# Kernel tuning notes

Hardware: AMD Instinct MI355X
Metric: run time of the kernel (lower is better)

Reference implementation:

```python
import jax, jax.numpy as jnp
import numpy as np

NUM_HEADS = 16
D_MODEL = 1024
HEAD_DIM = D_MODEL // NUM_HEADS
B, S = 2, 2048


def setup_inputs() -> dict:
    key = jax.random.key(0)
    ks = jax.random.split(key, 11)
    scale = 1.0 / np.sqrt(D_MODEL)
    inp = {
        'query': jax.random.normal(ks[0], (B, S, D_MODEL), jnp.float32),
        'key': jax.random.normal(ks[1], (B, S, D_MODEL), jnp.float32),
        'value': jax.random.normal(ks[2], (B, S, D_MODEL), jnp.float32),
        'Wq': jax.random.normal(ks[3], (D_MODEL, D_MODEL), jnp.float32) * scale,
        'bq': jnp.zeros((D_MODEL,), jnp.float32),
        'Wk': jax.random.normal(ks[4], (D_MODEL, D_MODEL), jnp.float32) * scale,
        'bk': jnp.zeros((D_MODEL,), jnp.float32),
        'Wv': jax.random.normal(ks[5], (D_MODEL, D_MODEL), jnp.float32) * scale,
        'bv': jnp.zeros((D_MODEL,), jnp.float32),
        'Wo': jax.random.normal(ks[6], (D_MODEL, D_MODEL), jnp.float32) * scale,
        'bo': jnp.zeros((D_MODEL,), jnp.float32),
    }
    return inp


def reference(query, key, value, Wq, bq, Wk, bk, Wv, bv, Wo, bo):
    b, s, _ = query.shape
    # Linear projections (torch Linear: x @ W.T + b; here W stored as [in,out])
    Q = query @ Wq + bq
    K = key @ Wk + bk
    V = value @ Wv + bv
    # [B, H, S, Dh]
    Q = Q.reshape(b, s, NUM_HEADS, HEAD_DIM).transpose(0, 2, 1, 3)
    K = K.reshape(b, -1, NUM_HEADS, HEAD_DIM).transpose(0, 2, 1, 3)
    V = V.reshape(b, -1, NUM_HEADS, HEAD_DIM).transpose(0, 2, 1, 3)
    scores = jnp.einsum('bhqd,bhkd->bhqk', Q, K) / jnp.sqrt(jnp.float32(HEAD_DIM)).astype(Q.dtype)
    attn = jax.nn.softmax(scores, axis=-1)
    ctx = jnp.einsum('bhqk,bhkd->bhqd', attn, V)
    ctx = ctx.transpose(0, 2, 1, 3).reshape(b, s, D_MODEL)
    return ctx @ Wo + bo
```

## Files before the change

kernel.cpp:

```cpp
#include <hip/hip_runtime.h>
#include <hip/hip_bf16.h>
#include <math.h>

#define NUM_HEADS 16
#define D_MODEL 1024
#define HEAD_DIM 64
#define BATCH 2
#define SEQ 2048
#define M_TOTAL (BATCH*SEQ)

typedef __bf16 bf16;
typedef __bf16 bf16x2 __attribute__((ext_vector_type(2)));
typedef __bf16 bf16x4 __attribute__((ext_vector_type(4)));
typedef __bf16 bf16x8 __attribute__((ext_vector_type(8)));
typedef float  floatx4 __attribute__((ext_vector_type(4)));

#define CLSCALE 0.180336884f

__device__ __forceinline__ void async_copy16(const bf16* g, bf16* l) {
    __builtin_amdgcn_global_load_lds(
        (const __attribute__((address_space(1))) void*)g,
        (__attribute__((address_space(3))) void*)l, 16, 0, 0);
}

__global__ __launch_bounds__(256)
void convert_w_kernel(const float* __restrict__ Wq, const float* __restrict__ Wk,
                      const float* __restrict__ Wv, const float* __restrict__ Wo,
                      bf16* __restrict__ Wt)
{
    const int z = blockIdx.z;
    const float* W = (z == 0) ? Wq : (z == 1) ? Wk : (z == 2) ? Wv : Wo;
    bf16* dstM = Wt + (size_t)z * D_MODEL * D_MODEL;

    const int n  = blockIdx.x * 256 + threadIdx.x;
    const int k0 = blockIdx.y * 64;
    bf16* dst = dstM + (size_t)n * D_MODEL + k0;

    #pragma unroll
    for (int jc = 0; jc < 8; ++jc) {
        bf16x8 w;
        #pragma unroll
        for (int j = 0; j < 8; ++j)
            w[j] = (bf16)W[(size_t)(k0 + jc * 8 + j) * D_MODEL + n];
        *(bf16x8*)(dst + jc * 8) = w;
    }
}

__global__ __launch_bounds__(256)
void convert_x_kernel(const float* __restrict__ q, const float* __restrict__ k,
                      const float* __restrict__ v, bf16* __restrict__ Xb)
{
    const int z = blockIdx.z;
    const float* X = (z == 0) ? q : (z == 1) ? k : v;
    bf16* dst = Xb + (size_t)z * M_TOTAL * D_MODEL;
    size_t i = ((size_t)blockIdx.x * 256 + threadIdx.x) * 8;
    const float4 u = *(const float4*)(X + i);
    const float4 w = *(const float4*)(X + i + 4);
    bf16x8 o;
    o[0] = (bf16)u.x; o[1] = (bf16)u.y; o[2] = (bf16)u.z; o[3] = (bf16)u.w;
    o[4] = (bf16)w.x; o[5] = (bf16)w.y; o[6] = (bf16)w.z; o[7] = (bf16)w.w;
    *(bf16x8*)(dst + i) = o;
}

__global__ __launch_bounds__(256)
void proj_kernel(const bf16* __restrict__ Xb, const bf16* __restrict__ Wt,
                 const float* __restrict__ bq, const float* __restrict__ bk,
                 const float* __restrict__ bv,
                 bf16* __restrict__ Qo, bf16* __restrict__ Ko, bf16* __restrict__ Vto)
{
    const int which = blockIdx.z;
    const bf16* X     = Xb + (size_t)which * M_TOTAL * D_MODEL;
    const bf16* Wm    = Wt + (size_t)which * D_MODEL * D_MODEL;
    const float* bias = (which == 0) ? bq : (which == 1) ? bk : bv;

    const int tileM = blockIdx.y * 128;
    const int tileN = blockIdx.x * 128;
    const int tid  = threadIdx.x;
    const int lane = tid & 63;
    const int wave = tid >> 6;
    const int quad = lane >> 4;
    const int l16  = lane & 15;

    __shared__ bf16 sA[128 * 32];
    __shared__ bf16 sB[128 * 32];

    floatx4 acc[4][4];
    const floatx4 z4 = {0.0f, 0.0f, 0.0f, 0.0f};
    #pragma unroll
    for (int i = 0; i < 4; i++)
        #pragma unroll
        for (int j = 0; j < 4; j++) acc[i][j] = z4;

    const int wm = (wave >> 1) * 64;
    const int wn = (wave & 1) * 64;

    const int c0   = wave * 64 + lane;
    const int row0 = c0 >> 2, col0 = (c0 & 3) * 8;
    const int c1   = c0 + 256;
    const int row1 = c1 >> 2, col1 = (c1 & 3) * 8;
    bf16* ldsA0 = sA + (size_t)(wave * 64) * 8;
    bf16* ldsA1 = sA + (size_t)(256 + wave * 64) * 8;
    bf16* ldsB0 = sB + (size_t)(wave * 64) * 8;
    bf16* ldsB1 = sB + (size_t)(256 + wave * 64) * 8;

    for (int k0 = 0; k0 < D_MODEL; k0 += 32) {
        __syncthreads();
        async_copy16(X  + (size_t)(tileM + row0) * D_MODEL + k0 + col0, ldsA0);
        async_copy16(X  + (size_t)(tileM + row1) * D_MODEL + k0 + col1, ldsA1);
        async_copy16(Wm + (size_t)(tileN + row0) * D_MODEL + k0 + col0, ldsB0);
        async_copy16(Wm + (size_t)(tileN + row1) * D_MODEL + k0 + col1, ldsB1);
        __syncthreads();

        bf16x8 af[4], bfr[4];
        #pragma unroll
        for (int i = 0; i < 4; i++) af[i]  = *(const bf16x8*)&sA[(wm + i * 16 + l16) * 32 + quad * 8];
        #pragma unroll
        for (int j = 0; j < 4; j++) bfr[j] = *(const bf16x8*)&sB[(wn + j * 16 + l16) * 32 + quad * 8];
        if (which != 2) {
            #pragma unroll
            for (int i = 0; i < 4; i++)
                #pragma unroll
                for (int j = 0; j < 4; j++)
                    acc[i][j] = __builtin_amdgcn_mfma_f32_16x16x32_bf16(af[i], bfr[j], acc[i][j], 0, 0, 0);
        } else {
            #pragma unroll
            for (int i = 0; i < 4; i++)
                #pragma unroll
                for (int j = 0; j < 4; j++)
                    acc[i][j] = __builtin_amdgcn_mfma_f32_16x16x32_bf16(bfr[i], af[j], acc[i][j], 0, 0, 0);
        }
    }

    if (which != 2) {
        bf16* out = (which == 0) ? Qo : Ko;
        const float oscale = (which == 0) ? CLSCALE : 1.0f;
        #pragma unroll
        for (int i = 0; i < 4; i++) {
            int mbase = tileM + wm + i * 16 + quad * 4;
            #pragma unroll
            for (int j = 0; j < 4; j++) {
                int n = tileN + wn + j * 16 + l16;
                float bb = bias[n];
                int h = n >> 6, d = n & 63;
                #pragma unroll
                for (int r = 0; r < 4; r++) {
                    int mm = mbase + r;
                    int b = mm >> 11, s = mm & 2047;
                    out[(((size_t)(b * NUM_HEADS + h)) * SEQ + s) * HEAD_DIM + d] =
                        (bf16)((acc[i][j][r] + bb) * oscale);
                }
            }
        }
    } else {
        #pragma unroll
        for (int i = 0; i < 4; i++) {
            #pragma unroll
            for (int r = 0; r < 4; r++) {
                int n = tileN + wn + i * 16 + quad * 4 + r;
                float bb = bias[n];
                int h = n >> 6, d = n & 63;
                #pragma unroll
                for (int j = 0; j < 4; j++) {
                    int m = tileM + wm + j * 16 + l16;
                    int b = m >> 11, s = m & 2047;
                    Vto[(((size_t)(b * NUM_HEADS + h)) * HEAD_DIM + d) * SEQ + s] =
                        (bf16)(acc[i][j][r] + bb);
                }
            }
        }
    }
}

__global__ __launch_bounds__(256)
void attn_kernel(const bf16* __restrict__ Q, const bf16* __restrict__ K,
                 const bf16* __restrict__ Vt, bf16* __restrict__ Ctx)
{
    const int bh  = blockIdx.y;
    const int b   = bh >> 4, h = bh & 15;
    const int q0  = blockIdx.x * 128;
    const int tid = threadIdx.x;
    const int lane = tid & 63;
    const int wave = tid >> 6;
    const int quad = lane >> 4;
    const int l16  = lane & 15;

    __shared__ bf16 sQP[128][72];
    __shared__ bf16 sK[64][72];
    __shared__ bf16 sVt[64][72];

    const bf16* Qb  = Q  + ((size_t)bh * SEQ + q0) * HEAD_DIM;
    const bf16* Kb  = K  + (size_t)bh * SEQ * HEAD_DIM;
    const bf16* Vtb = Vt + (size_t)bh * HEAD_DIM * SEQ;

    #pragma unroll
    for (int it = 0; it < 4; ++it) {
        int g   = tid + it * 256;
        int row = g >> 3;
        int c   = (g & 7) * 8;
        *(bf16x8*)&sQP[row][c] = *(const bf16x8*)(Qb + (size_t)row * HEAD_DIM + c);
    }
    __syncthreads();

    const int wq = wave * 32;
    bf16x8 bQ[2][2];
    #pragma unroll
    for (int qt = 0; qt < 2; qt++) {
        bQ[qt][0] = *(const bf16x8*)&sQP[wq + qt * 16 + l16][quad * 8];
        bQ[qt][1] = *(const bf16x8*)&sQP[wq + qt * 16 + l16][32 + quad * 8];
    }

    floatx4 o[2][4];
    const floatx4 z4 = {0.0f, 0.0f, 0.0f, 0.0f};
    #pragma unroll
    for (int qt = 0; qt < 2; qt++)
        #pragma unroll
        for (int t = 0; t < 4; t++) o[qt][t] = z4;
    floatx4 lpart[2] = {z4, z4};

    for (int kt = 0; kt < SEQ / 64; ++kt) {
        __syncthreads();
        #pragma unroll
        for (int it = 0; it < 2; ++it) {
            int g   = tid + it * 256;
            int row = g >> 3;
            int c   = (g & 7) * 8;
            *(bf16x8*)&sK[row][c] =
                *(const bf16x8*)(Kb + ((size_t)(kt * 64 + row)) * HEAD_DIM + c);
        }
        #pragma unroll
        for (int it = 0; it < 2; ++it) {
            int g = tid + it * 256;
            int d = g >> 3;
            int c = (g & 7) * 8;
            *(bf16x8*)&sVt[d][c] =
                *(const bf16x8*)(Vtb + (size_t)d * SEQ + kt * 64 + c);
        }
        __syncthreads();

        floatx4 sc[2][4];
        #pragma unroll
        for (int t = 0; t < 4; t++) {
            bf16x8 a0 = *(const bf16x8*)&sK[t * 16 + l16][quad * 8];
            bf16x8 a1 = *(const bf16x8*)&sK[t * 16 + l16][32 + quad * 8];
            #pragma unroll
            for (int qt = 0; qt < 2; qt++) {
                floatx4 z = z4;
                z = __builtin_amdgcn_mfma_f32_16x16x32_bf16(a0, bQ[qt][0], z, 0, 0, 0);
                z = __builtin_amdgcn_mfma_f32_16x16x32_bf16(a1, bQ[qt][1], z, 0, 0, 0);
                sc[qt][t] = z;
            }
        }

        #pragma unroll
        for (int qt = 0; qt < 2; qt++) {
            #pragma unroll
            for (int t = 0; t < 4; t++)
                #pragma unroll
                for (int r = 0; r < 4; r++)
                    sc[qt][t][r] = exp2f(sc[qt][t][r]);
            lpart[qt] += sc[qt][0] + sc[qt][1] + sc[qt][2] + sc[qt][3];
        }

        #pragma unroll
        for (int qt = 0; qt < 2; qt++)
            #pragma unroll
            for (int t = 0; t < 4; t++) {
                bf16x4 pk;
                #pragma unroll
                for (int r = 0; r < 4; r++) pk[r] = (bf16)sc[qt][t][r];
                *(bf16x4*)&sQP[wq + qt * 16 + l16][t * 16 + quad * 4] = pk;
            }

        bf16x8 bP[2][2];
        #pragma unroll
        for (int qt = 0; qt < 2; qt++) {
            bP[qt][0] = *(const bf16x8*)&sQP[wq + qt * 16 + l16][quad * 8];
            bP[qt][1] = *(const bf16x8*)&sQP[wq + qt * 16 + l16][32 + quad * 8];
        }

        #pragma unroll
        for (int dt = 0; dt < 4; dt++) {
            bf16x8 a0 = *(const bf16x8*)&sVt[dt * 16 + l16][quad * 8];
            bf16x8 a1 = *(const bf16x8*)&sVt[dt * 16 + l16][32 + quad * 8];
            #pragma unroll
            for (int qt = 0; qt < 2; qt++) {
                o[qt][dt] = __builtin_amdgcn_mfma_f32_16x16x32_bf16(a0, bP[qt][0], o[qt][dt], 0, 0, 0);
                o[qt][dt] = __builtin_amdgcn_mfma_f32_16x16x32_bf16(a1, bP[qt][1], o[qt][dt], 0, 0, 0);
            }
        }
    }

    #pragma unroll
    for (int qt = 0; qt < 2; qt++) {
        float rs = (lpart[qt][0] + lpart[qt][1]) + (lpart[qt][2] + lpart[qt][3]);
        rs += __shfl_xor(rs, 16, 64);
        rs += __shfl_xor(rs, 32, 64);
        float inv = 1.0f / rs;

        int q = q0 + wq + qt * 16 + l16;
        size_t base = ((size_t)b * SEQ + q) * D_MODEL + h * HEAD_DIM;
        #pragma unroll
        for (int dt = 0; dt < 4; dt++) {
            bf16x4 w;
            #pragma unroll
            for (int r = 0; r < 4; r++) w[r] = (bf16)(o[qt][dt][r] * inv);
            *(bf16x4*)&Ctx[base + dt * 16 + quad * 4] = w;
        }
    }
}

__global__ __launch_bounds__(256)
void out_proj_kernel(const bf16* __restrict__ A, const bf16* __restrict__ Wto,
                     const float* __restrict__ bias, float* __restrict__ Out)
{
    const int tileM = blockIdx.y * 64;
    const int tileN = blockIdx.x * 128;
    const int tid  = threadIdx.x;
    const int lane = tid & 63;
    const int wave = tid >> 6;
    const int quad = lane >> 4;
    const int l16  = lane & 15;

    __shared__ bf16 sA[64 * 32];
    __shared__ bf16 sB[128 * 32];

    floatx4 acc[2][4];
    const floatx4 z4 = {0.0f, 0.0f, 0.0f, 0.0f};
    #pragma unroll
    for (int i = 0; i < 2; i++)
        #pragma unroll
        for (int j = 0; j < 4; j++) acc[i][j] = z4;

    const int wm = (wave >> 1) * 32;
    const int wn = (wave & 1) * 64;

    const int c0   = wave * 64 + lane;
    const int row0 = c0 >> 2, col0 = (c0 & 3) * 8;
    const int c1   = c0 + 256;
    const int row1 = c1 >> 2, col1 = (c1 & 3) * 8;
    bf16* ldsA0 = sA + (size_t)(wave * 64) * 8;
    bf16* ldsB0 = sB + (size_t)(wave * 64) * 8;
    bf16* ldsB1 = sB + (size_t)(256 + wave * 64) * 8;

    for (int k0 = 0; k0 < D_MODEL; k0 += 32) {
        __syncthreads();
        async_copy16(A   + (size_t)(tileM + row0) * D_MODEL + k0 + col0, ldsA0);
        async_copy16(Wto + (size_t)(tileN + row0) * D_MODEL + k0 + col0, ldsB0);
        async_copy16(Wto + (size_t)(tileN + row1) * D_MODEL + k0 + col1, ldsB1);
        __syncthreads();

        bf16x8 af[2], bfr[4];
        #pragma unroll
        for (int i = 0; i < 2; i++) af[i]  = *(const bf16x8*)&sA[(wm + i * 16 + l16) * 32 + quad * 8];
        #pragma unroll
        for (int j = 0; j < 4; j++) bfr[j] = *(const bf16x8*)&sB[(wn + j * 16 + l16) * 32 + quad * 8];
        #pragma unroll
        for (int i = 0; i < 2; i++)
            #pragma unroll
            for (int j = 0; j < 4; j++)
                acc[i][j] = __builtin_amdgcn_mfma_f32_16x16x32_bf16(af[i], bfr[j], acc[i][j], 0, 0, 0);
    }

    #pragma unroll
    for (int i = 0; i < 2; i++) {
        int mbase = tileM + wm + i * 16 + quad * 4;
        #pragma unroll
        for (int j = 0; j < 4; j++) {
            int n = tileN + wn + j * 16 + l16;
            float bb = bias[n];
            #pragma unroll
            for (int r = 0; r < 4; r++)
                Out[(size_t)(mbase + r) * D_MODEL + n] = acc[i][j][r] + bb;
        }
    }
}

extern "C" void kernel_launch(void* const* d_in, const int* in_sizes, int n_in,
                              void* d_out, int out_size, void* d_ws, size_t ws_size,
                              hipStream_t stream)
{
    const float* q  = (const float*)d_in[0];
    const float* k  = (const float*)d_in[1];
    const float* v  = (const float*)d_in[2];
    const float* Wq = (const float*)d_in[3];
    const float* bq = (const float*)d_in[4];
    const float* Wk = (const float*)d_in[5];
    const float* bk = (const float*)d_in[6];
    const float* Wv = (const float*)d_in[7];
    const float* bv = (const float*)d_in[8];
    const float* Wo = (const float*)d_in[9];
    const float* bo = (const float*)d_in[10];
    float* out = (float*)d_out;

    const size_t PLANE = (size_t)M_TOTAL * D_MODEL;
    bf16* Qb = (bf16*)d_ws;
    bf16* Kb = Qb + PLANE;
    bf16* Vt = Kb + PLANE;
    bf16* Cb = Vt + PLANE;
    bf16* Wt = Cb + PLANE;
    bf16* Xb = Wt + 4 * (size_t)D_MODEL * D_MODEL;

    convert_w_kernel<<<dim3(4, 16, 4), 256, 0, stream>>>(Wq, Wk, Wv, Wo, Wt);
    convert_x_kernel<<<dim3(2048, 1, 3), 256, 0, stream>>>(q, k, v, Xb);
    proj_kernel<<<dim3(8, 32, 3), 256, 0, stream>>>(Xb, Wt, bq, bk, bv, Qb, Kb, Vt);
    attn_kernel<<<dim3(16, 32), 256, 0, stream>>>(Qb, Kb, Vt, Cb);
    out_proj_kernel<<<dim3(8, 64), 256, 0, stream>>>(Cb, Wt + 3 * (size_t)D_MODEL * D_MODEL, bo, out);
}
```

Measured before the change: 272.9 us.

## Use async global-to-LDS loads with XOR swizzle and smaller attention blocks

The attention kernel now runs 64 query rows per block with 128 threads, doubling the grid to 1024 blocks. K and V tiles are loaded with direct global-to-LDS async copies into unpadded, XOR-swizzled shared buffers, and the MFMA operand reads use matching swizzled offsets. The aim is to drop the register round-trip on tile loads, avoid LDS bank conflicts without padding, and raise occupancy and block count. The trade-off is that each block reuses every K/V tile for half as many queries, so global traffic for K/V doubles. Correctness also depends on the async copies being complete at the following barrier.

```diff
diff --git a/kernel.cpp b/kernel.cpp
--- a/kernel.cpp
+++ b/kernel.cpp
@@ -171,22 +171,22 @@
     }
 }
 
-__global__ __launch_bounds__(256)
+__global__ __launch_bounds__(128)
 void attn_kernel(const bf16* __restrict__ Q, const bf16* __restrict__ K,
                  const bf16* __restrict__ Vt, bf16* __restrict__ Ctx)
 {
     const int bh  = blockIdx.y;
     const int b   = bh >> 4, h = bh & 15;
-    const int q0  = blockIdx.x * 128;
+    const int q0  = blockIdx.x * 64;
     const int tid = threadIdx.x;
     const int lane = tid & 63;
     const int wave = tid >> 6;
     const int quad = lane >> 4;
     const int l16  = lane & 15;
 
-    __shared__ bf16 sQP[128][72];
-    __shared__ bf16 sK[64][72];
-    __shared__ bf16 sVt[64][72];
+    __shared__ bf16 sQP[64][72];
+    __shared__ bf16 sK[64 * 64];
+    __shared__ bf16 sVt[64 * 64];
 
     const bf16* Qb  = Q  + ((size_t)bh * SEQ + q0) * HEAD_DIM;
     const bf16* Kb  = K  + (size_t)bh * SEQ * HEAD_DIM;
@@ -194,7 +194,7 @@
 
     #pragma unroll
     for (int it = 0; it < 4; ++it) {
-        int g   = tid + it * 256;
+        int g   = tid + it * 128;
         int row = g >> 3;
         int c   = (g & 7) * 8;
         *(bf16x8*)&sQP[row][c] = *(const bf16x8*)(Qb + (size_t)row * HEAD_DIM + c);
@@ -217,31 +217,30 @@
         for (int t = 0; t < 4; t++) o[qt][t] = z4;
     floatx4 lpart[2] = {z4, z4};
 
+    const int xs = l16 & 7;
+    const int cho0 = ((quad)     ^ xs) * 8;
+    const int cho1 = ((4 + quad) ^ xs) * 8;
+
     for (int kt = 0; kt < SEQ / 64; ++kt) {
         __syncthreads();
         #pragma unroll
-        for (int it = 0; it < 2; ++it) {
-            int g   = tid + it * 256;
-            int row = g >> 3;
-            int c   = (g & 7) * 8;
-            *(bf16x8*)&sK[row][c] =
-                *(const bf16x8*)(Kb + ((size_t)(kt * 64 + row)) * HEAD_DIM + c);
-        }
-        #pragma unroll
-        for (int it = 0; it < 2; ++it) {
-            int g = tid + it * 256;
-            int d = g >> 3;
-            int c = (g & 7) * 8;
-            *(bf16x8*)&sVt[d][c] =
-                *(const bf16x8*)(Vtb + (size_t)d * SEQ + kt * 64 + c);
+        for (int it = 0; it < 4; ++it) {
+            int c    = tid + it * 128;
+            int row  = c >> 3;
+            int scol = ((c & 7) ^ (row & 7)) * 8;
+            async_copy16(Kb  + (size_t)(kt * 64 + row) * HEAD_DIM + scol,
+                         sK + (size_t)c * 8);
+            async_copy16(Vtb + (size_t)row * SEQ + kt * 64 + scol,
+                         sVt + (size_t)c * 8);
         }
         __syncthreads();
 
         floatx4 sc[2][4];
         #pragma unroll
         for (int t = 0; t < 4; t++) {
-            bf16x8 a0 = *(const bf16x8*)&sK[t * 16 + l16][quad * 8];
-            bf16x8 a1 = *(const bf16x8*)&sK[t * 16 + l16][32 + quad * 8];
+            const int ra = (t * 16 + l16) * 64;
+            bf16x8 a0 = *(const bf16x8*)&sK[ra + cho0];
+            bf16x8 a1 = *(const bf16x8*)&sK[ra + cho1];
             #pragma unroll
             for (int qt = 0; qt < 2; qt++) {
                 floatx4 z = z4;
@@ -280,8 +279,9 @@
 
         #pragma unroll
         for (int dt = 0; dt < 4; dt++) {
-            bf16x8 a0 = *(const bf16x8*)&sVt[dt * 16 + l16][quad * 8];
-            bf16x8 a1 = *(const bf16x8*)&sVt[dt * 16 + l16][32 + quad * 8];
+            const int ra = (dt * 16 + l16) * 64;
+            bf16x8 a0 = *(const bf16x8*)&sVt[ra + cho0];
+            bf16x8 a1 = *(const bf16x8*)&sVt[ra + cho1];
             #pragma unroll
             for (int qt = 0; qt < 2; qt++) {
                 o[qt][dt] = __builtin_amdgcn_mfma_f32_16x16x32_bf16(a0, bP[qt][0], o[qt][dt], 0, 0, 0);
@@ -403,6 +403,6 @@
     convert_w_kernel<<<dim3(4, 16, 4), 256, 0, stream>>>(Wq, Wk, Wv, Wo, Wt);
     convert_x_kernel<<<dim3(2048, 1, 3), 256, 0, stream>>>(q, k, v, Xb);
     proj_kernel<<<dim3(8, 32, 3), 256, 0, stream>>>(Xb, Wt, bq, bk, bv, Qb, Kb, Vt);
-    attn_kernel<<<dim3(16, 32), 256, 0, stream>>>(Qb, Kb, Vt, Cb);
+    attn_kernel<<<dim3(32, 32), 128, 0, stream>>>(Qb, Kb, Vt, Cb);
     out_proj_kernel<<<dim3(8, 64), 256, 0, stream>>>(Cb, Wt + 3 * (size_t)D_MODEL * D_MODEL, bo, out);
 }
```

New measurement: 271.7 us. No clear change (-0.4%).
